# Kernel optimization log

Measured on AMD Instinct MI355X. Metric: run time of the kernel, lower is better.

Reference implementation:

```python
import jax, jax.numpy as jnp
import numpy as np

RADIUS = 0.2
K = 32  # num_neighbors


def setup_inputs() -> dict:
    key = jax.random.key(0)
    k1, k2, k3 = jax.random.split(key, 3)
    points_xyz = jax.random.uniform(k1, (2, 16384, 3), dtype=jnp.float32)
    center_xyz = jax.random.uniform(k2, (2, 2048, 3), dtype=jnp.float32)
    features = jax.random.normal(k3, (2, 64, 16384), dtype=jnp.float32)
    return {"points_xyz": points_xyz, "center_xyz": center_xyz, "features": features}


def _ball_query(center_xyz, points_xyz, k, radius):
    # squared distances (B, G, N) via ||c||^2 + ||p||^2 - 2 c.p (avoids (B,G,N,3) temp)
    c2 = jnp.sum(center_xyz * center_xyz, axis=-1)  # (B, G)
    p2 = jnp.sum(points_xyz * points_xyz, axis=-1)  # (B, N)
    cp = jnp.einsum('bgd,bnd->bgn', center_xyz, points_xyz)
    d2 = c2[:, :, None] + p2[:, None, :] - 2.0 * cp  # (B, G, N)
    n = points_xyz.shape[1]
    # key = point index if inside ball else sentinel N; first-K-in-ball == K smallest keys
    keys = jnp.where(d2 < radius * radius, jnp.arange(n, dtype=jnp.int32), n)
    neg_vals, _ = jax.lax.top_k(-keys, k)
    idx = -neg_vals  # (B, G, K) ascending point indices, sentinel n if <k found
    first = idx[..., :1]
    # pad missing slots with first found index (CUDA ball_query semantics), 0 if none
    idx = jnp.where(idx < n, idx, jnp.where(first < n, first, 0))
    return idx


def reference(points_xyz, center_xyz, features):
    idx = _ball_query(center_xyz, points_xyz, K, RADIUS)  # (B, G, K) int32
    gather = jax.vmap(lambda f, i: f[:, i])  # (C, N), (G, K) -> (C, G, K)
    grouped_xyz = gather(jnp.swapaxes(points_xyz, 1, 2), idx)  # (B, 3, G, K)
    # relative_xyz then normalize_xyz
    grouped_xyz = (grouped_xyz - jnp.swapaxes(center_xyz, 1, 2)[..., None]) / RADIUS
    grouped_features = gather(features, idx)  # (B, C, G, K)
    return grouped_xyz, grouped_features
```

## Files before the change

### kernel.cpp

```cpp
#include <hip/hip_runtime.h>
#include <hip/hip_bf16.h>

constexpr int NPTS = 16384;
constexpr int NCTR = 2048;
constexpr int NCH  = 64;
constexpr int KK   = 32;
constexpr int NB   = 2;
#define R2 0.04f

__global__ __launch_bounds__(256) void prep_kernel(
    const float* __restrict__ points,
    const float* __restrict__ feats,
    float* __restrict__ featsT,
    float4* __restrict__ packed)
{
#pragma clang fp contract(off)
    __shared__ float tile[64][65];

    if (blockIdx.x < 512) {
        const int b  = blockIdx.x >> 8;
        const int n0 = (blockIdx.x & 255) * 64;
        const int t  = threadIdx.x;
        const int nl = t & 63;
        const int q  = t >> 6;

        const float* fb = feats + (size_t)b * NCH * NPTS;
#pragma unroll
        for (int r = 0; r < 16; ++r) {
            int c = r * 4 + q;
            tile[c][nl] = fb[(size_t)c * NPTS + n0 + nl];
        }
        __syncthreads();
        float* ftb = featsT + ((size_t)b * NPTS + n0) * NCH;
#pragma unroll
        for (int r = 0; r < 16; ++r) {
            int n = r * 4 + q;
            ftb[(size_t)n * NCH + nl] = tile[nl][n];
        }
        return;
    }

    const int tid = (blockIdx.x - 512) * 256 + threadIdx.x;
#pragma unroll
    for (int s = 0; s < 4; ++s) {
        const int i = tid + s * 8192;
        const float x = points[3 * i + 0];
        const float y = points[3 * i + 1];
        const float z = points[3 * i + 2];
        const float p2 = (x * x + y * y) + z * z;
        packed[i] = make_float4(x, y, z, p2);
    }
}

__global__ __launch_bounds__(256, 4) void query_group(
    const float4* __restrict__ packed,
    const float* __restrict__ centers,
    const float* __restrict__ featsT,
    float* __restrict__ out_xyz,
    float* __restrict__ out_feat)
{
#pragma clang fp contract(off)
    __shared__ int   s_idx[4][KK];
    __shared__ float s_f[4][KK][68];

    const int wave = threadIdx.x >> 6;
    const int lane = threadIdx.x & 63;
    const int cg   = blockIdx.x * 4 + wave;
    const int b    = cg >> 11;
    const int g    = cg & (NCTR - 1);

    const float4* pk = packed + (size_t)b * NPTS;
    const float* cc = centers + (size_t)cg * 3;
    const float cx = cc[0], cy = cc[1], cz = cc[2];
    const float c2 = (cx * cx + cy * cy) + cz * cz;

    int* idxs = s_idx[wave];

    float4 cur[8], nxt[8];
#pragma unroll
    for (int j = 0; j < 8; ++j) cur[j] = pk[j * 64 + lane];
    int cnt = 0;
    for (int base = 0; base < NPTS; base += 512) {
        const int nbb = (base + 512 < NPTS) ? base + 512 : 0;
#pragma unroll
        for (int j = 0; j < 8; ++j) nxt[j] = pk[nbb + j * 64 + lane];
#pragma unroll
        for (int j = 0; j < 8; ++j) {
            const float4 v = cur[j];
            const float cp = (cx * v.x + cy * v.y) + cz * v.z;
            const float d2 = (c2 + v.w) - 2.0f * cp;
            const bool hit = d2 < R2;
            const unsigned long long m = __ballot(hit);
            if (hit) {
                const int slot = cnt + __popcll(m & ((1ull << lane) - 1ull));
                if (slot < KK) idxs[slot] = base + j * 64 + lane;
            }
            cnt += (int)__popcll(m);
        }
        if (cnt >= KK) break;
#pragma unroll
        for (int j = 0; j < 8; ++j) cur[j] = nxt[j];
    }
    __syncthreads();

    const int cpd = cnt < KK ? cnt : KK;
    const int first = (cnt > 0) ? idxs[0] : 0;
    if (lane < KK) {
        const int id = (lane < cpd) ? idxs[lane] : first;
        idxs[lane] = id;
        const float4 v = pk[id];
        const size_t ob = (((size_t)b * 3 + 0) * NCTR + g) * KK + lane;
        out_xyz[ob + (size_t)0 * NCTR * KK] = (v.x - cx) / 0.2f;
        out_xyz[ob + (size_t)1 * NCTR * KK] = (v.y - cy) / 0.2f;
        out_xyz[ob + (size_t)2 * NCTR * KK] = (v.z - cz) / 0.2f;
    }
    __syncthreads();

    float (*sf)[68] = s_f[wave];
    const int li = lane & 15, r = lane >> 4;
    const float* ftb = featsT + (size_t)b * NPTS * NCH;
#pragma unroll
    for (int i = 0; i < 8; ++i) {
        const int k = i * 4 + r;
        const float4 v = *((const float4*)(ftb + (size_t)idxs[k] * NCH) + li);
        *(float4*)&sf[k][4 * li] = v;
    }
    __syncthreads();

    const int kq = lane & 7;
    const int c0 = lane >> 3;
    const size_t ob = ((size_t)b * NCH * NCTR + g) * KK;
#pragma unroll
    for (int p = 0; p < 8; ++p) {
        const int c = c0 + 8 * p;
        float4 v;
        v.x = sf[4 * kq + 0][c];
        v.y = sf[4 * kq + 1][c];
        v.z = sf[4 * kq + 2][c];
        v.w = sf[4 * kq + 3][c];
        *(float4*)(out_feat + ob + (size_t)c * NCTR * KK + 4 * kq) = v;
    }
}

__global__ __launch_bounds__(256) void ballquery_group(
    const float* __restrict__ points, const float* __restrict__ centers,
    const float* __restrict__ feats, float* __restrict__ out_xyz,
    float* __restrict__ out_feat)
{
#pragma clang fp contract(off)
    __shared__ int   s_idx[4][KK];
    __shared__ float s_f[4][KK][65];
    const int wave = threadIdx.x >> 6, lane = threadIdx.x & 63;
    const int cg = blockIdx.x * 4 + wave;
    const int b = cg >> 11, g = cg & (NCTR - 1);
    const float* pb = points + (size_t)b * NPTS * 3;
    const float* cc = centers + (size_t)cg * 3;
    const float cx = cc[0], cy = cc[1], cz = cc[2];
    const float c2 = (cx * cx + cy * cy) + cz * cz;
    int* idxs = s_idx[wave];
    int cnt = 0;
    for (int base = 0; base < NPTS; base += 64) {
        const int i = base + lane;
        const float px = pb[i * 3 + 0], py = pb[i * 3 + 1], pz = pb[i * 3 + 2];
        const float p2 = (px * px + py * py) + pz * pz;
        const float cp = (cx * px + cy * py) + cz * pz;
        const float d2 = (c2 + p2) - 2.0f * cp;
        const bool hit = d2 < R2;
        const unsigned long long m = __ballot(hit);
        if (hit) {
            const int slot = cnt + __popcll(m & ((1ull << lane) - 1ull));
            if (slot < KK) idxs[slot] = i;
        }
        cnt += (int)__popcll(m);
        if (cnt >= KK) break;
    }
    __syncthreads();
    const int cpd = cnt < KK ? cnt : KK;
    const int first = (cnt > 0) ? idxs[0] : 0;
    if (lane < KK) idxs[lane] = (lane < cpd) ? idxs[lane] : first;
    __syncthreads();
    if (lane < KK) {
        const int id = idxs[lane];
        const float px = pb[id * 3 + 0], py = pb[id * 3 + 1], pz = pb[id * 3 + 2];
        const size_t ob = (((size_t)b * 3 + 0) * NCTR + g) * KK + lane;
        out_xyz[ob + (size_t)0 * NCTR * KK] = (px - cx) / 0.2f;
        out_xyz[ob + (size_t)1 * NCTR * KK] = (py - cy) / 0.2f;
        out_xyz[ob + (size_t)2 * NCTR * KK] = (pz - cz) / 0.2f;
    }
    float (*sf)[65] = s_f[wave];
    const float* fb = feats + (size_t)b * NCH * NPTS;
    for (int k = 0; k < KK; ++k) {
        const int id = idxs[k];
        sf[k][lane] = fb[(size_t)lane * NPTS + id];
    }
    __syncthreads();
    const int k = lane & 31, ch = lane >> 5;
    const size_t ob = ((size_t)b * NCH * NCTR + g) * KK;
#pragma unroll
    for (int cc2 = 0; cc2 < 32; ++cc2) {
        const int c = cc2 * 2 + ch;
        out_feat[ob + (size_t)c * NCTR * KK + k] = sf[k][c];
    }
}

extern "C" void kernel_launch(void* const* d_in, const int* in_sizes, int n_in,
                              void* d_out, int out_size, void* d_ws, size_t ws_size,
                              hipStream_t stream) {
    const float* points  = (const float*)d_in[0];
    const float* centers = (const float*)d_in[1];
    const float* feats   = (const float*)d_in[2];

    float* out      = (float*)d_out;
    float* out_xyz  = out;
    float* out_feat = out + (size_t)NB * 3 * NCTR * KK;

    const size_t ftBytes = (size_t)NB * NPTS * NCH * sizeof(float);
    const size_t pkBytes = (size_t)NB * NPTS * 4 * sizeof(float);

    if (ws_size >= ftBytes + pkBytes) {
        float*  featsT = (float*)d_ws;
        float4* packed = (float4*)((char*)d_ws + ftBytes);
        prep_kernel<<<544, 256, 0, stream>>>(points, feats, featsT, packed);
        query_group<<<(NB * NCTR) / 4, 256, 0, stream>>>(
            packed, centers, featsT, out_xyz, out_feat);
    } else {
        ballquery_group<<<(NB * NCTR) / 4, 256, 0, stream>>>(
            points, centers, feats, out_xyz, out_feat);
    }
}
```

Measured before the change: 87.90 us.

## Replace feature transpose with per-channel LDS row gather kernel

Removes the prep kernel that transposed features and packed points. The query kernel now reads raw xyz and computes p2 inline, then writes neighbor indices to workspace. A new gather kernel loads one whole feature channel row (64KB) into LDS per block and serves the gathers for a quarter of the centers from LDS, writing coalesced float4 outputs. This drops the full feature transpose write and re-read, in exchange for reloading each channel row four times and using large LDS allocations that limit occupancy.

```diff
diff --git a/kernel.cpp b/kernel.cpp
--- a/kernel.cpp
+++ b/kernel.cpp
@@ -1,5 +1,4 @@
 #include <hip/hip_runtime.h>
-#include <hip/hip_bf16.h>
 
 constexpr int NPTS = 16384;
 constexpr int NCTR = 2048;
@@ -8,87 +7,50 @@
 constexpr int NB   = 2;
 #define R2 0.04f
 
-__global__ __launch_bounds__(256) void prep_kernel(
+__global__ __launch_bounds__(256, 4) void query_kernel(
     const float* __restrict__ points,
-    const float* __restrict__ feats,
-    float* __restrict__ featsT,
-    float4* __restrict__ packed)
+    const float* __restrict__ centers,
+    float* __restrict__ out_xyz,
+    int* __restrict__ idx_out)
 {
 #pragma clang fp contract(off)
-    __shared__ float tile[64][65];
-
-    if (blockIdx.x < 512) {
-        const int b  = blockIdx.x >> 8;
-        const int n0 = (blockIdx.x & 255) * 64;
-        const int t  = threadIdx.x;
-        const int nl = t & 63;
-        const int q  = t >> 6;
-
-        const float* fb = feats + (size_t)b * NCH * NPTS;
-#pragma unroll
-        for (int r = 0; r < 16; ++r) {
-            int c = r * 4 + q;
-            tile[c][nl] = fb[(size_t)c * NPTS + n0 + nl];
-        }
-        __syncthreads();
-        float* ftb = featsT + ((size_t)b * NPTS + n0) * NCH;
-#pragma unroll
-        for (int r = 0; r < 16; ++r) {
-            int n = r * 4 + q;
-            ftb[(size_t)n * NCH + nl] = tile[nl][n];
-        }
-        return;
-    }
-
-    const int tid = (blockIdx.x - 512) * 256 + threadIdx.x;
-#pragma unroll
-    for (int s = 0; s < 4; ++s) {
-        const int i = tid + s * 8192;
-        const float x = points[3 * i + 0];
-        const float y = points[3 * i + 1];
-        const float z = points[3 * i + 2];
-        const float p2 = (x * x + y * y) + z * z;
-        packed[i] = make_float4(x, y, z, p2);
-    }
-}
-
-__global__ __launch_bounds__(256, 4) void query_group(
-    const float4* __restrict__ packed,
-    const float* __restrict__ centers,
-    const float* __restrict__ featsT,
-    float* __restrict__ out_xyz,
-    float* __restrict__ out_feat)
-{
-#pragma clang fp contract(off)
-    __shared__ int   s_idx[4][KK];
-    __shared__ float s_f[4][KK][68];
-
+    __shared__ int s_idx[4][KK];
     const int wave = threadIdx.x >> 6;
     const int lane = threadIdx.x & 63;
     const int cg   = blockIdx.x * 4 + wave;
     const int b    = cg >> 11;
     const int g    = cg & (NCTR - 1);
 
-    const float4* pk = packed + (size_t)b * NPTS;
+    const float* pb = points + (size_t)b * NPTS * 3;
     const float* cc = centers + (size_t)cg * 3;
     const float cx = cc[0], cy = cc[1], cz = cc[2];
     const float c2 = (cx * cx + cy * cy) + cz * cz;
-
     int* idxs = s_idx[wave];
 
-    float4 cur[8], nxt[8];
-#pragma unroll
-    for (int j = 0; j < 8; ++j) cur[j] = pk[j * 64 + lane];
+    float curx[8], cury[8], curz[8], nxx[8], nxy[8], nxz[8];
+#pragma unroll
+    for (int j = 0; j < 8; ++j) {
+        const int i = j * 64 + lane;
+        curx[j] = pb[3 * i + 0];
+        cury[j] = pb[3 * i + 1];
+        curz[j] = pb[3 * i + 2];
+    }
     int cnt = 0;
     for (int base = 0; base < NPTS; base += 512) {
         const int nbb = (base + 512 < NPTS) ? base + 512 : 0;
 #pragma unroll
-        for (int j = 0; j < 8; ++j) nxt[j] = pk[nbb + j * 64 + lane];
-#pragma unroll
         for (int j = 0; j < 8; ++j) {
-            const float4 v = cur[j];
-            const float cp = (cx * v.x + cy * v.y) + cz * v.z;
-            const float d2 = (c2 + v.w) - 2.0f * cp;
+            const int i = nbb + j * 64 + lane;
+            nxx[j] = pb[3 * i + 0];
+            nxy[j] = pb[3 * i + 1];
+            nxz[j] = pb[3 * i + 2];
+        }
+#pragma unroll
+        for (int j = 0; j < 8; ++j) {
+            const float x = curx[j], y = cury[j], z = curz[j];
+            const float p2 = (x * x + y * y) + z * z;
+            const float cp = (cx * x + cy * y) + cz * z;
+            const float d2 = (c2 + p2) - 2.0f * cp;
             const bool hit = d2 < R2;
             const unsigned long long m = __ballot(hit);
             if (hit) {
@@ -99,7 +61,9 @@
         }
         if (cnt >= KK) break;
 #pragma unroll
-        for (int j = 0; j < 8; ++j) cur[j] = nxt[j];
+        for (int j = 0; j < 8; ++j) {
+            curx[j] = nxx[j]; cury[j] = nxy[j]; curz[j] = nxz[j];
+        }
     }
     __syncthreads();
 
@@ -107,38 +71,47 @@
     const int first = (cnt > 0) ? idxs[0] : 0;
     if (lane < KK) {
         const int id = (lane < cpd) ? idxs[lane] : first;
-        idxs[lane] = id;
-        const float4 v = pk[id];
+        idx_out[(size_t)cg * KK + lane] = id;
+        const float vx = pb[3 * id + 0];
+        const float vy = pb[3 * id + 1];
+        const float vz = pb[3 * id + 2];
         const size_t ob = (((size_t)b * 3 + 0) * NCTR + g) * KK + lane;
-        out_xyz[ob + (size_t)0 * NCTR * KK] = (v.x - cx) / 0.2f;
-        out_xyz[ob + (size_t)1 * NCTR * KK] = (v.y - cy) / 0.2f;
-        out_xyz[ob + (size_t)2 * NCTR * KK] = (v.z - cz) / 0.2f;
-    }
-    __syncthreads();
-
-    float (*sf)[68] = s_f[wave];
-    const int li = lane & 15, r = lane >> 4;
-    const float* ftb = featsT + (size_t)b * NPTS * NCH;
-#pragma unroll
-    for (int i = 0; i < 8; ++i) {
-        const int k = i * 4 + r;
-        const float4 v = *((const float4*)(ftb + (size_t)idxs[k] * NCH) + li);
-        *(float4*)&sf[k][4 * li] = v;
-    }
-    __syncthreads();
-
-    const int kq = lane & 7;
-    const int c0 = lane >> 3;
-    const size_t ob = ((size_t)b * NCH * NCTR + g) * KK;
-#pragma unroll
-    for (int p = 0; p < 8; ++p) {
-        const int c = c0 + 8 * p;
+        out_xyz[ob + (size_t)0 * NCTR * KK] = (vx - cx) / 0.2f;
+        out_xyz[ob + (size_t)1 * NCTR * KK] = (vy - cy) / 0.2f;
+        out_xyz[ob + (size_t)2 * NCTR * KK] = (vz - cz) / 0.2f;
+    }
+}
+
+__global__ __launch_bounds__(256, 2) void gather_kernel(
+    const float* __restrict__ feats,
+    const int* __restrict__ idx,
+    float* __restrict__ out_feat)
+{
+    __shared__ float sRow[NPTS];
+    const int wid = ((int)blockIdx.x % 8) * 64 + (int)blockIdx.x / 8;
+    const int q = wid & 3;
+    const int c = (wid >> 2) & 63;
+    const int b = wid >> 8;
+    const int t = threadIdx.x;
+
+    const float4* rowV = (const float4*)(feats + ((size_t)b * NCH + c) * NPTS);
+    float4* sV = (float4*)sRow;
+#pragma unroll
+    for (int it = 0; it < 16; ++it) sV[it * 256 + t] = rowV[it * 256 + t];
+    __syncthreads();
+
+    const int4* idxQ = (const int4*)(idx + ((size_t)b * NCTR + q * 512) * KK);
+    float4* outQ = (float4*)(out_feat + (((size_t)b * NCH + c) * NCTR + q * 512) * KK);
+#pragma unroll
+    for (int it = 0; it < 16; ++it) {
+        const int o = it * 256 + t;
+        const int4 id4 = idxQ[o];
         float4 v;
-        v.x = sf[4 * kq + 0][c];
-        v.y = sf[4 * kq + 1][c];
-        v.z = sf[4 * kq + 2][c];
-        v.w = sf[4 * kq + 3][c];
-        *(float4*)(out_feat + ob + (size_t)c * NCTR * KK + 4 * kq) = v;
+        v.x = sRow[id4.x];
+        v.y = sRow[id4.y];
+        v.z = sRow[id4.z];
+        v.w = sRow[id4.w];
+        outQ[o] = v;
     }
 }
 
@@ -214,15 +187,14 @@
     float* out_xyz  = out;
     float* out_feat = out + (size_t)NB * 3 * NCTR * KK;
 
-    const size_t ftBytes = (size_t)NB * NPTS * NCH * sizeof(float);
-    const size_t pkBytes = (size_t)NB * NPTS * 4 * sizeof(float);
-
-    if (ws_size >= ftBytes + pkBytes) {
-        float*  featsT = (float*)d_ws;
-        float4* packed = (float4*)((char*)d_ws + ftBytes);
-        prep_kernel<<<544, 256, 0, stream>>>(points, feats, featsT, packed);
-        query_group<<<(NB * NCTR) / 4, 256, 0, stream>>>(
-            packed, centers, featsT, out_xyz, out_feat);
+    const size_t idxBytes = (size_t)NB * NCTR * KK * sizeof(int);
+
+    if (ws_size >= idxBytes) {
+        int* idx_ws = (int*)d_ws;
+        query_kernel<<<(NB * NCTR) / 4, 256, 0, stream>>>(
+            points, centers, out_xyz, idx_ws);
+        gather_kernel<<<NB * NCH * 4, 256, 0, stream>>>(
+            feats, idx_ws, out_feat);
     } else {
         ballquery_group<<<(NB * NCTR) / 4, 256, 0, stream>>>(
             points, centers, feats, out_xyz, out_feat);
```

After: 88.92 us. No clear change (+1.2%).
